# Optimization experiments

Hardware: AMD Instinct MI355X
Metric: run time of the kernel (lower is better)

Reference implementation:

```python
import jax, jax.numpy as jnp
import numpy as np

D_MODEL, D_STATE, D_CONV, EXPAND = 1024, 16, 4, 2
D_INNER = D_MODEL * EXPAND
BATCH, SEQ = 2, 2048


def setup_inputs() -> dict:
    key = jax.random.key(0)
    ks = jax.random.split(key, 10)
    s = lambda *sh: 1.0 / np.sqrt(sh[-1])
    x = jax.random.normal(ks[0], (BATCH, SEQ, D_MODEL), jnp.float32)
    W_in = jax.random.normal(ks[1], (2 * D_INNER, D_MODEL), jnp.float32) * s(D_MODEL)
    conv_w = jax.random.normal(ks[2], (D_INNER, 1, D_CONV), jnp.float32) * s(D_CONV)
    conv_b = jax.random.normal(ks[3], (D_INNER,), jnp.float32) * 0.01
    W_x = jax.random.normal(ks[4], (2 * D_STATE + 1, D_INNER), jnp.float32) * s(D_INNER)
    W_dt = jax.random.normal(ks[5], (D_INNER, 1), jnp.float32)
    b_dt = jax.random.normal(ks[6], (D_INNER,), jnp.float32) * 0.01
    A_log = jnp.log(jnp.broadcast_to(jnp.arange(1, D_STATE + 1, dtype=jnp.float32), (D_INNER, D_STATE)))
    D = jnp.ones((D_INNER,), jnp.float32)
    W_out = jax.random.normal(ks[7], (D_MODEL, D_INNER), jnp.float32) * s(D_INNER)
    return {"x": x, "W_in": W_in, "conv_w": conv_w, "conv_b": conv_b,
            "W_x": W_x, "W_dt": W_dt, "b_dt": b_dt, "A_log": A_log, "D": D, "W_out": W_out}


def _selective_ssm(x, W_in, conv_w, conv_b, W_x, W_dt, b_dt, A_log, D, W_out):
    B_, L, _ = x.shape
    d_inner = conv_w.shape[0]
    d_conv = conv_w.shape[-1]
    d_state = A_log.shape[-1]
    # input projection -> (x, z), each [B, L, d_inner]
    xz = jnp.einsum('bld,ed->ble', x, W_in)
    xi, z = jnp.split(xz, 2, axis=-1)
    # depthwise causal conv over time (torch pads both sides then slices [:L] == left-pad)
    x_ncl = jnp.moveaxis(xi, 1, 2)  # [B, d_inner, L]
    x_conv = jax.lax.conv_general_dilated(
        x_ncl, conv_w, window_strides=(1,), padding=[(d_conv - 1, 0)],
        dimension_numbers=('NCH', 'OIH', 'NCH'), feature_group_count=d_inner)
    x_conv = x_conv + conv_b[None, :, None]
    xi = jax.nn.silu(jnp.moveaxis(x_conv, 1, 2))  # [B, L, d_inner]
    # selective parameters
    x_dbl = jnp.einsum('bld,ed->ble', xi, W_x)  # [B, L, 2*d_state+1]
    dt_raw = x_dbl[..., :1]
    Bmat = x_dbl[..., 1:1 + d_state]
    Cmat = x_dbl[..., 1 + d_state:]
    dt = jax.nn.softplus(dt_raw * W_dt[None, None, :, 0] + b_dt)  # [B, L, d_inner]
    A = -jnp.exp(A_log)  # [d_inner, d_state]
    # recurrence: h_t = exp(dt_t*A)*h_{t-1} + (dt_t*B_t)*x_t ; y_t = <h_t, C_t>
    def step(h, inp):
        x_t, dt_t, B_t, C_t = inp  # [B,d], [B,d], [B,n], [B,n]
        dA = jnp.exp(dt_t[..., None] * A)              # [B, d, n]
        dB = dt_t[..., None] * B_t[:, None, :]          # [B, d, n]
        h = dA * h + dB * x_t[..., None]
        y = jnp.einsum('bdn,bn->bd', h, C_t)
        return h, y

    h0 = jnp.zeros((B_, d_inner, d_state), xi.dtype)
    xs = (jnp.moveaxis(xi, 0, 1), jnp.moveaxis(dt, 0, 1),
          jnp.moveaxis(Bmat, 0, 1), jnp.moveaxis(Cmat, 0, 1))
    _, ys = jax.lax.scan(step, h0, xs)                 # [L, B, d_inner]
    y = jnp.moveaxis(ys, 0, 1) + D * xi                # skip term D*x_t
    y = y * jax.nn.silu(z)
    return jnp.einsum('bld,ed->ble', y, W_out)


def reference(x, W_in, conv_w, conv_b, W_x, W_dt, b_dt, A_log, D, W_out):
    return _selective_ssm(x, W_in, conv_w, conv_b, W_x, W_dt, b_dt, A_log, D, W_out)
```

## Files before the change

### kernel.cpp

```cpp
#include <hip/hip_runtime.h>
#include <hip/hip_bf16.h>

#define D_MODEL 1024
#define D_STATE 16
#define D_CONV  4
#define D_INNER 2048
#define BATCH   2
#define SEQ     2048
#define NTOK    (BATCH * SEQ)
#define NXZ     (2 * D_INNER)
#define NDBL    (2 * D_STATE + 1)
#define XROW    40
#define CHUNK   32
#define NCHUNK  (SEQ / CHUNK)

typedef __attribute__((ext_vector_type(8))) short bf16x8;
typedef __attribute__((ext_vector_type(4))) float f32x4;

__device__ __forceinline__ float silu_fast(float x) {
    return x / (1.0f + __expf(-x));
}
__device__ __forceinline__ float softplus_fast(float x) {
    float r = __logf(1.0f + __expf(x));
    return (x > 20.f) ? x : r;
}
__device__ __forceinline__ short f2bf(float f) {
    __hip_bfloat16 h = __float2bfloat16(f);
    return __builtin_bit_cast(short, h);
}
__device__ __forceinline__ float bf2f(short s) {
    return __bfloat162float(__builtin_bit_cast(__hip_bfloat16, s));
}
__device__ __forceinline__ void gload_lds16(const void* g, void* l) {
    __builtin_amdgcn_global_load_lds(
        (const __attribute__((address_space(1))) void*)g,
        (__attribute__((address_space(3))) void*)l, 16, 0, 0);
}

__global__ void split_kernel(const float* __restrict__ in, short* __restrict__ hi,
                             short* __restrict__ lo, int n4)
{
    int i = blockIdx.x * blockDim.x + threadIdx.x;
    if (i >= n4) return;
    float4 v = ((const float4*)in)[i];
    short4 h, l;
    h.x = f2bf(v.x); l.x = f2bf(v.x - bf2f(h.x));
    h.y = f2bf(v.y); l.y = f2bf(v.y - bf2f(h.y));
    h.z = f2bf(v.z); l.z = f2bf(v.z - bf2f(h.z));
    h.w = f2bf(v.w); l.w = f2bf(v.w - bf2f(h.w));
    ((short4*)hi)[i] = h;
    ((short4*)lo)[i] = l;
}

__launch_bounds__(256, 2)
__global__ void mfma_gemm_split(const short* __restrict__ Ahi, const short* __restrict__ Alo,
                                const short* __restrict__ Bhi, const short* __restrict__ Blo,
                                float* __restrict__ C, int M, int N, int K)
{
    __shared__ short sAh[4096], sAl[4096], sBh[4096], sBl[4096];
    const int tid  = threadIdx.x;
    const int lane = tid & 63;
    const int wave = tid >> 6;
    const int bm = blockIdx.y, bn = blockIdx.x;
    const int wm = wave >> 1, wn = wave & 1;

    const int r0a = bm * 128, r0b = bn * 128;

    f32x4 acc[4][4] = {};

    for (int k0 = 0; k0 < K; k0 += 32) {
        __syncthreads();
#pragma unroll
        for (int i = 0; i < 2; ++i) {
            const int off = i * 4096 + tid * 16;
            const int g   = off >> 11;
            const int row = (off >> 4) & 127;
            const size_t ea = (size_t)(r0a + row) * K + k0 + g * 8;
            const size_t eb = (size_t)(r0b + row) * K + k0 + g * 8;
            char* la = (char*)sAh + i * 4096 + wave * 1024;
            gload_lds16(Ahi + ea, la);
            gload_lds16(Alo + ea, (char*)sAl + i * 4096 + wave * 1024);
            gload_lds16(Bhi + eb, (char*)sBh + i * 4096 + wave * 1024);
            gload_lds16(Blo + eb, (char*)sBl + i * 4096 + wave * 1024);
        }
        __syncthreads();

        const int g = lane >> 4;
        bf16x8 ah[4], al[4], bh[4], bl[4];
#pragma unroll
        for (int m = 0; m < 4; ++m) {
            const int rowA = wm * 64 + m * 16 + (lane & 15);
            const int rowB = wn * 64 + m * 16 + (lane & 15);
            ah[m] = ((const bf16x8*)sAh)[g * 128 + rowA];
            al[m] = ((const bf16x8*)sAl)[g * 128 + rowA];
            bh[m] = ((const bf16x8*)sBh)[g * 128 + rowB];
            bl[m] = ((const bf16x8*)sBl)[g * 128 + rowB];
        }
#pragma unroll
        for (int m = 0; m < 4; ++m)
#pragma unroll
            for (int n = 0; n < 4; ++n) {
                acc[m][n] = __builtin_amdgcn_mfma_f32_16x16x32_bf16(ah[m], bh[n], acc[m][n], 0, 0, 0);
                acc[m][n] = __builtin_amdgcn_mfma_f32_16x16x32_bf16(ah[m], bl[n], acc[m][n], 0, 0, 0);
                acc[m][n] = __builtin_amdgcn_mfma_f32_16x16x32_bf16(al[m], bh[n], acc[m][n], 0, 0, 0);
            }
    }

#pragma unroll
    for (int m = 0; m < 4; ++m) {
        const int row = bm * 128 + wm * 64 + m * 16 + ((lane >> 4) << 2);
#pragma unroll
        for (int n = 0; n < 4; ++n) {
            const int col = bn * 128 + wn * 64 + n * 16 + (lane & 15);
#pragma unroll
            for (int r = 0; r < 4; ++r)
                C[(size_t)(row + r) * N + col] = acc[m][n][r];
        }
    }
}

__global__ void conv_silu_kernel(const float* __restrict__ xz,
                                 const float* __restrict__ conv_w,
                                 const float* __restrict__ conv_b,
                                 float* __restrict__ xi)
{
    int idx = blockIdx.x * blockDim.x + threadIdx.x;
    if (idx >= NTOK * D_INNER) return;
    int d = idx % D_INNER;
    int t = idx / D_INNER;
    int l = t % SEQ;
    int b = t / SEQ;

    float w0 = conv_w[d * 4 + 0], w1 = conv_w[d * 4 + 1];
    float w2 = conv_w[d * 4 + 2], w3 = conv_w[d * 4 + 3];

    const float* base = xz + ((size_t)b * SEQ) * NXZ + d;
    float acc = conv_b[d];
    if (l >= 3) acc = fmaf(w0, base[(size_t)(l - 3) * NXZ], acc);
    if (l >= 2) acc = fmaf(w1, base[(size_t)(l - 2) * NXZ], acc);
    if (l >= 1) acc = fmaf(w2, base[(size_t)(l - 1) * NXZ], acc);
    acc = fmaf(w3, base[(size_t)l * NXZ], acc);
    xi[idx] = silu_fast(acc);
}

__launch_bounds__(256)
__global__ void xdbl_kernel(const float* __restrict__ xi,
                            const float* __restrict__ W_x,
                            float* __restrict__ xdbl)
{
    __shared__ float row[D_INNER];
    const int t = blockIdx.x;
    const float* xr = xi + (size_t)t * D_INNER;
    for (int i = threadIdx.x; i < D_INNER; i += 256) row[i] = xr[i];
    __syncthreads();

    const int wave = threadIdx.x >> 6;
    const int lane = threadIdx.x & 63;
    for (int e = wave; e < NDBL; e += 4) {
        const float* wr = W_x + (size_t)e * D_INNER;
        float s = 0.f;
        for (int i = lane; i < D_INNER; i += 64) s = fmaf(row[i], wr[i], s);
#pragma unroll
        for (int off = 32; off; off >>= 1) s += __shfl_xor(s, off);
        if (lane == 0) xdbl[(size_t)t * XROW + (e == 0 ? 0 : e + 3)] = s;
    }
}

__launch_bounds__(256)
__global__ void scan_pass1(const float* __restrict__ xdbl,
                           const float* __restrict__ xi,
                           const float* __restrict__ W_dt,
                           const float* __restrict__ b_dt,
                           const float* __restrict__ A_log,
                           float* __restrict__ aprod,
                           float* __restrict__ hloc)
{
    const int d = blockIdx.x * 256 + threadIdx.x;
    const int c = blockIdx.y;
    const int b = blockIdx.z;

    float A[16];
    {
        const float4* ar = (const float4*)(A_log + (size_t)d * 16);
#pragma unroll
        for (int q = 0; q < 4; ++q) {
            float4 v = ar[q];
            A[q * 4 + 0] = -__expf(v.x);
            A[q * 4 + 1] = -__expf(v.y);
            A[q * 4 + 2] = -__expf(v.z);
            A[q * 4 + 3] = -__expf(v.w);
        }
    }
    const float wdt = W_dt[d], bdt = b_dt[d];

    const float* xd = xdbl + ((size_t)b * SEQ + c * CHUNK) * XROW;
    const float* xp = xi + ((size_t)b * SEQ + c * CHUNK) * D_INNER + d;

    float h[16], ap[16], Bv[16];
#pragma unroll
    for (int n = 0; n < 16; ++n) { h[n] = 0.f; ap[n] = 1.f; }

    for (int l = 0; l < CHUNK; ++l) {
        float raw = xd[0];
#pragma unroll
        for (int q = 0; q < 4; ++q) {
            float4 v = *(const float4*)(xd + 4 + q * 4);
            Bv[q * 4 + 0] = v.x; Bv[q * 4 + 1] = v.y;
            Bv[q * 4 + 2] = v.z; Bv[q * 4 + 3] = v.w;
        }
        float xv = xp[0];
        float dtv = softplus_fast(fmaf(raw, wdt, bdt));
        float dtx = dtv * xv;
#pragma unroll
        for (int n = 0; n < 16; ++n) {
            float e = __expf(dtv * A[n]);
            h[n]  = fmaf(e, h[n], Bv[n] * dtx);
            ap[n] *= e;
        }
        xd += XROW; xp += D_INNER;
    }

    size_t s = (((size_t)b * NCHUNK + c) * D_INNER + d) * 16;
#pragma unroll
    for (int q = 0; q < 4; ++q) {
        *(float4*)(aprod + s + q * 4) = make_float4(ap[q*4], ap[q*4+1], ap[q*4+2], ap[q*4+3]);
        *(float4*)(hloc  + s + q * 4) = make_float4(h[q*4],  h[q*4+1],  h[q*4+2],  h[q*4+3]);
    }
}

__global__ void scan_combine(float* __restrict__ aprod,
                             const float* __restrict__ hloc)
{
    int idx = blockIdx.x * blockDim.x + threadIdx.x;
    int b  = idx >> 15;
    int dn = idx & 32767;
    float hs = 0.f;
#pragma unroll
    for (int c = 0; c < NCHUNK; ++c) {
        size_t s = (((size_t)b * NCHUNK + c) << 15) + dn;
        float ap = aprod[s];
        float hl = hloc[s];
        aprod[s] = hs;
        hs = fmaf(ap, hs, hl);
    }
}

__launch_bounds__(256)
__global__ void scan_pass2(const float* __restrict__ xdbl,
                           float* __restrict__ xi,
                           const float* __restrict__ xz,
                           const float* __restrict__ W_dt,
                           const float* __restrict__ b_dt,
                           const float* __restrict__ A_log,
                           const float* __restrict__ Dvec,
                           const float* __restrict__ hstart)
{
    const int d = blockIdx.x * 256 + threadIdx.x;
    const int c = blockIdx.y;
    const int b = blockIdx.z;

    float A[16];
    {
        const float4* ar = (const float4*)(A_log + (size_t)d * 16);
#pragma unroll
        for (int q = 0; q < 4; ++q) {
            float4 v = ar[q];
            A[q * 4 + 0] = -__expf(v.x);
            A[q * 4 + 1] = -__expf(v.y);
            A[q * 4 + 2] = -__expf(v.z);
            A[q * 4 + 3] = -__expf(v.w);
        }
    }
    const float wdt = W_dt[d], bdt = b_dt[d], Dd = Dvec[d];

    const float* xd = xdbl + ((size_t)b * SEQ + c * CHUNK) * XROW;
    float*       xp = xi + ((size_t)b * SEQ + c * CHUNK) * D_INNER + d;
    const float* zp = xz + ((size_t)b * SEQ + c * CHUNK) * NXZ + D_INNER + d;

    float h[16], Bv[16], Cv[16];
    {
        size_t s = (((size_t)b * NCHUNK + c) * D_INNER + d) * 16;
#pragma unroll
        for (int q = 0; q < 4; ++q) {
            float4 v = *(const float4*)(hstart + s + q * 4);
            h[q * 4 + 0] = v.x; h[q * 4 + 1] = v.y;
            h[q * 4 + 2] = v.z; h[q * 4 + 3] = v.w;
        }
    }

    for (int l = 0; l < CHUNK; ++l) {
        float raw = xd[0];
#pragma unroll
        for (int q = 0; q < 4; ++q) {
            float4 v = *(const float4*)(xd + 4 + q * 4);
            Bv[q * 4 + 0] = v.x; Bv[q * 4 + 1] = v.y;
            Bv[q * 4 + 2] = v.z; Bv[q * 4 + 3] = v.w;
            float4 w = *(const float4*)(xd + 20 + q * 4);
            Cv[q * 4 + 0] = w.x; Cv[q * 4 + 1] = w.y;
            Cv[q * 4 + 2] = w.z; Cv[q * 4 + 3] = w.w;
        }
        float xv = xp[0];
        float zv = zp[0];
        float dtv = softplus_fast(fmaf(raw, wdt, bdt));
        float dtx = dtv * xv;

        float p0 = 0.f, p1 = 0.f, p2 = 0.f, p3 = 0.f;
#pragma unroll
        for (int q = 0; q < 4; ++q) {
            float e0 = __expf(dtv * A[q*4+0]);
            float e1 = __expf(dtv * A[q*4+1]);
            float e2 = __expf(dtv * A[q*4+2]);
            float e3 = __expf(dtv * A[q*4+3]);
            h[q*4+0] = fmaf(e0, h[q*4+0], Bv[q*4+0] * dtx);
            h[q*4+1] = fmaf(e1, h[q*4+1], Bv[q*4+1] * dtx);
            h[q*4+2] = fmaf(e2, h[q*4+2], Bv[q*4+2] * dtx);
            h[q*4+3] = fmaf(e3, h[q*4+3], Bv[q*4+3] * dtx);
            p0 = fmaf(h[q*4+0], Cv[q*4+0], p0);
            p1 = fmaf(h[q*4+1], Cv[q*4+1], p1);
            p2 = fmaf(h[q*4+2], Cv[q*4+2], p2);
            p3 = fmaf(h[q*4+3], Cv[q*4+3], p3);
        }
        float y = (p0 + p1) + (p2 + p3) + Dd * xv;
        xp[0] = y * silu_fast(zv);

        xd += XROW; xp += D_INNER; zp += NXZ;
    }
}

extern "C" void kernel_launch(void* const* d_in, const int* in_sizes, int n_in,
                              void* d_out, int out_size, void* d_ws, size_t ws_size,
                              hipStream_t stream)
{
    (void)in_sizes; (void)n_in; (void)out_size; (void)ws_size;

    const float* x      = (const float*)d_in[0];
    const float* W_in   = (const float*)d_in[1];
    const float* conv_w = (const float*)d_in[2];
    const float* conv_b = (const float*)d_in[3];
    const float* W_x    = (const float*)d_in[4];
    const float* W_dt   = (const float*)d_in[5];
    const float* b_dt   = (const float*)d_in[6];
    const float* A_log  = (const float*)d_in[7];
    const float* Dvec   = (const float*)d_in[8];
    const float* W_out  = (const float*)d_in[9];
    float* out = (float*)d_out;

    float* xz   = (float*)d_ws;
    float* xi   = xz + (size_t)NTOK * NXZ;
    float* xdbl = xi + (size_t)NTOK * D_INNER;
    float* R    = xdbl + (size_t)NTOK * XROW;

    short* x_hi   = (short*)R;
    short* x_lo   = x_hi + (size_t)NTOK * D_MODEL;
    short* Win_hi = x_lo + (size_t)NTOK * D_MODEL;
    short* Win_lo = Win_hi + (size_t)NXZ * D_MODEL;
    float* aprod  = R;
    float* hloc   = aprod + (size_t)BATCH * NCHUNK * D_INNER * 16;
    short* y_hi   = (short*)xz;
    short* y_lo   = y_hi + (size_t)NTOK * D_INNER;
    short* Wou_hi = y_lo + (size_t)NTOK * D_INNER;
    short* Wou_lo = Wou_hi + (size_t)D_MODEL * D_INNER;

    split_kernel<<<(NTOK * D_MODEL / 4 + 255) / 256, 256, 0, stream>>>(x, x_hi, x_lo, NTOK * D_MODEL / 4);
    split_kernel<<<(NXZ * D_MODEL / 4 + 255) / 256, 256, 0, stream>>>(W_in, Win_hi, Win_lo, NXZ * D_MODEL / 4);

    {
        dim3 grid(NXZ / 128, NTOK / 128);
        mfma_gemm_split<<<grid, 256, 0, stream>>>(x_hi, x_lo, Win_hi, Win_lo, xz, NTOK, NXZ, D_MODEL);
    }
    {
        int total = NTOK * D_INNER;
        conv_silu_kernel<<<(total + 255) / 256, 256, 0, stream>>>(xz, conv_w, conv_b, xi);
    }
    xdbl_kernel<<<NTOK, 256, 0, stream>>>(xi, W_x, xdbl);

    {
        dim3 grid(D_INNER / 256, NCHUNK, BATCH);
        scan_pass1<<<grid, 256, 0, stream>>>(xdbl, xi, W_dt, b_dt, A_log, aprod, hloc);
        scan_combine<<<(BATCH * D_INNER * 16) / 256, 256, 0, stream>>>(aprod, hloc);
        scan_pass2<<<grid, 256, 0, stream>>>(xdbl, xi, xz, W_dt, b_dt, A_log, Dvec, aprod);
    }
    split_kernel<<<(NTOK * D_INNER / 4 + 255) / 256, 256, 0, stream>>>(xi, y_hi, y_lo, NTOK * D_INNER / 4);
    split_kernel<<<(D_MODEL * D_INNER / 4 + 255) / 256, 256, 0, stream>>>(W_out, Wou_hi, Wou_lo, D_MODEL * D_INNER / 4);
    {
        dim3 grid(D_MODEL / 128, NTOK / 128);
        mfma_gemm_split<<<grid, 256, 0, stream>>>(y_hi, y_lo, Wou_hi, Wou_lo, out, NTOK, D_MODEL, D_INNER);
    }
}
```

Measured before the change: 656.7 us.

## Overlap next-tile LDS staging with MFMA in split GEMM and batch xdbl tokens

The split-bf16 GEMM now issues the async global-to-LDS loads for the next K tile right after the current tile's fragments are read into registers, so the loads run while the MFMAs compute. Its launch bound is raised to three blocks per SM. The xdbl projection now handles four tokens per block and reuses each W_x load across four accumulators, which quarters W_x traffic and the number of blocks. In exchange the GEMM uses a single LDS buffer with an extra barrier per iteration, the tighter register limit may cause spills, and xdbl needs four times the shared memory per block.

```diff
diff --git a/kernel.cpp b/kernel.cpp
--- a/kernel.cpp
+++ b/kernel.cpp
@@ -13,6 +13,7 @@
 #define XROW    40
 #define CHUNK   32
 #define NCHUNK  (SEQ / CHUNK)
+#define XT      4
 
 typedef __attribute__((ext_vector_type(8))) short bf16x8;
 typedef __attribute__((ext_vector_type(4))) float f32x4;
@@ -52,7 +53,7 @@
     ((short4*)lo)[i] = l;
 }
 
-__launch_bounds__(256, 2)
+__launch_bounds__(256, 3)
 __global__ void mfma_gemm_split(const short* __restrict__ Ahi, const short* __restrict__ Alo,
                                 const short* __restrict__ Bhi, const short* __restrict__ Blo,
                                 float* __restrict__ C, int M, int N, int K)
@@ -66,10 +67,7 @@
 
     const int r0a = bm * 128, r0b = bn * 128;
 
-    f32x4 acc[4][4] = {};
-
-    for (int k0 = 0; k0 < K; k0 += 32) {
-        __syncthreads();
+    auto stage = [&](int k0) {
 #pragma unroll
         for (int i = 0; i < 2; ++i) {
             const int off = i * 4096 + tid * 16;
@@ -77,12 +75,17 @@
             const int row = (off >> 4) & 127;
             const size_t ea = (size_t)(r0a + row) * K + k0 + g * 8;
             const size_t eb = (size_t)(r0b + row) * K + k0 + g * 8;
-            char* la = (char*)sAh + i * 4096 + wave * 1024;
-            gload_lds16(Ahi + ea, la);
+            gload_lds16(Ahi + ea, (char*)sAh + i * 4096 + wave * 1024);
             gload_lds16(Alo + ea, (char*)sAl + i * 4096 + wave * 1024);
             gload_lds16(Bhi + eb, (char*)sBh + i * 4096 + wave * 1024);
             gload_lds16(Blo + eb, (char*)sBl + i * 4096 + wave * 1024);
         }
+    };
+
+    f32x4 acc[4][4] = {};
+
+    stage(0);
+    for (int k0 = 0; k0 < K; k0 += 32) {
         __syncthreads();
 
         const int g = lane >> 4;
@@ -96,6 +99,10 @@
             bh[m] = ((const bf16x8*)sBh)[g * 128 + rowB];
             bl[m] = ((const bf16x8*)sBl)[g * 128 + rowB];
         }
+        __syncthreads();
+
+        if (k0 + 32 < K) stage(k0 + 32);
+
 #pragma unroll
         for (int m = 0; m < 4; ++m)
 #pragma unroll
@@ -148,21 +155,38 @@
                             const float* __restrict__ W_x,
                             float* __restrict__ xdbl)
 {
-    __shared__ float row[D_INNER];
-    const int t = blockIdx.x;
-    const float* xr = xi + (size_t)t * D_INNER;
-    for (int i = threadIdx.x; i < D_INNER; i += 256) row[i] = xr[i];
+    __shared__ float rows[XT][D_INNER];
+    const int t0 = blockIdx.x * XT;
+    for (int i = threadIdx.x; i < XT * D_INNER; i += 256)
+        rows[i >> 11][i & 2047] = xi[(size_t)(t0 + (i >> 11)) * D_INNER + (i & 2047)];
     __syncthreads();
 
     const int wave = threadIdx.x >> 6;
     const int lane = threadIdx.x & 63;
     for (int e = wave; e < NDBL; e += 4) {
         const float* wr = W_x + (size_t)e * D_INNER;
-        float s = 0.f;
-        for (int i = lane; i < D_INNER; i += 64) s = fmaf(row[i], wr[i], s);
-#pragma unroll
-        for (int off = 32; off; off >>= 1) s += __shfl_xor(s, off);
-        if (lane == 0) xdbl[(size_t)t * XROW + (e == 0 ? 0 : e + 3)] = s;
+        float s0 = 0.f, s1 = 0.f, s2 = 0.f, s3 = 0.f;
+        for (int i = lane; i < D_INNER; i += 64) {
+            float w = wr[i];
+            s0 = fmaf(rows[0][i], w, s0);
+            s1 = fmaf(rows[1][i], w, s1);
+            s2 = fmaf(rows[2][i], w, s2);
+            s3 = fmaf(rows[3][i], w, s3);
+        }
+#pragma unroll
+        for (int off = 32; off; off >>= 1) {
+            s0 += __shfl_xor(s0, off);
+            s1 += __shfl_xor(s1, off);
+            s2 += __shfl_xor(s2, off);
+            s3 += __shfl_xor(s3, off);
+        }
+        if (lane == 0) {
+            const int slot = (e == 0 ? 0 : e + 3);
+            xdbl[(size_t)(t0 + 0) * XROW + slot] = s0;
+            xdbl[(size_t)(t0 + 1) * XROW + slot] = s1;
+            xdbl[(size_t)(t0 + 2) * XROW + slot] = s2;
+            xdbl[(size_t)(t0 + 3) * XROW + slot] = s3;
+        }
     }
 }
 
@@ -372,7 +396,7 @@
         int total = NTOK * D_INNER;
         conv_silu_kernel<<<(total + 255) / 256, 256, 0, stream>>>(xz, conv_w, conv_b, xi);
     }
-    xdbl_kernel<<<NTOK, 256, 0, stream>>>(xi, W_x, xdbl);
+    xdbl_kernel<<<NTOK / XT, 256, 0, stream>>>(xi, W_x, xdbl);
 
     {
         dim3 grid(D_INNER / 256, NCHUNK, BATCH);
```

Result: faster. 595.7 us (-9.3%).
